# Kernel tuning notes

Hardware: AMD Instinct MI355X
Metric: run time of the kernel (lower is better)

The kernel has to match this reference:

```python
import jax, jax.numpy as jnp
import numpy as np

NW = 64        # n_waveshapers
CE = 128       # control_embedding_size
W = 16         # shaping_fn_size (width)
OC = 1         # out_channels
EPS = 1e-5
SLOPE = 0.01   # LeakyReLU negative slope


def _layer_norm_c(x, g, b):
    # layer norm over channel axis of [B, C, T] (TimeDistributedLayerNorm)
    mu = jnp.mean(x, axis=1, keepdims=True)
    var = jnp.var(x, axis=1, keepdims=True)
    xn = (x - mu) * jax.lax.rsqrt(var + EPS)
    return xn * g[None, :, None] + b[None, :, None]


def _linear_interp(x, out_len):
    # torch F.interpolate(mode='linear', align_corners=False) on [B, C, L]
    L = x.shape[-1]
    scale = L / out_len
    pos = (jnp.arange(out_len, dtype=x.dtype) + 0.5) * scale - 0.5
    pos = jnp.clip(pos, 0.0, L - 1)
    i0 = jnp.floor(pos).astype(jnp.int32)
    i1 = jnp.minimum(i0 + 1, L - 1)
    frac = (pos - i0.astype(x.dtype))
    return x[..., i0] * (1.0 - frac) + x[..., i1] * frac


def setup_inputs() -> dict:
    key = jax.random.key(0)
    ks = jax.random.split(key, 32)
    B, T, TC = 4, 65536, 1024
    s_ce = 1.0 / np.sqrt(CE)
    inp = {
        'exciter': jax.random.normal(ks[0], (B, NW, T), jnp.float32),
        'control_embedding': jax.random.normal(ks[1], (B, CE, TC), jnp.float32),
        # TimeDistributedMLP (depth=4): three CE->CE convs + final CE->4*NW
        'mlp_w0': jax.random.normal(ks[2], (CE, CE), jnp.float32) * s_ce,
        'mlp_b0': jnp.zeros((CE,), jnp.float32),
        'ln0_g': jnp.ones((CE,), jnp.float32),
        'ln0_b': jnp.zeros((CE,), jnp.float32),
        'mlp_w1': jax.random.normal(ks[3], (CE, CE), jnp.float32) * s_ce,
        'mlp_b1': jnp.zeros((CE,), jnp.float32),
        'ln1_g': jnp.ones((CE,), jnp.float32),
        'ln1_b': jnp.zeros((CE,), jnp.float32),
        'mlp_w2': jax.random.normal(ks[4], (CE, CE), jnp.float32) * s_ce,
        'mlp_b2': jnp.zeros((CE,), jnp.float32),
        'ln2_g': jnp.ones((CE,), jnp.float32),
        'ln2_b': jnp.zeros((CE,), jnp.float32),
        'mlp_w3': jax.random.normal(ks[5], (4 * NW, CE), jnp.float32) * s_ce,
        'mlp_b3': jnp.zeros((4 * NW,), jnp.float32),
        # TrainableNonlinearity: input_scale + grouped k=1 convs (per-channel MLPs)
        'input_scale': jax.random.normal(ks[6], (1, NW, 1), jnp.float32) * 10.0,
        'sf_w0': jax.random.normal(ks[7], (NW, W), jnp.float32),            # 1 -> W per group
        'sf_b0': jnp.zeros((NW, W), jnp.float32),
        'sf_w1': jax.random.normal(ks[8], (NW, W, W), jnp.float32) / np.sqrt(W),  # W -> W per group
        'sf_b1': jnp.zeros((NW, W), jnp.float32),
        'sf_w2': jax.random.normal(ks[9], (NW, W), jnp.float32) / np.sqrt(W),     # W -> 1 per group
        'sf_b2': jnp.zeros((NW,), jnp.float32),
        # mixer conv1d NW -> OC, k=1
        'mix_w': jax.random.normal(ks[10], (OC, NW), jnp.float32) / np.sqrt(NW),
        'mix_b': jnp.zeros((OC,), jnp.float32),
    }
    return inp


def reference(exciter, control_embedding,
              mlp_w0, mlp_b0, ln0_g, ln0_b,
              mlp_w1, mlp_b1, ln1_g, ln1_b,
              mlp_w2, mlp_b2, ln2_g, ln2_b,
              mlp_w3, mlp_b3,
              input_scale, sf_w0, sf_b0, sf_w1, sf_b1, sf_w2, sf_b2,
              mix_w, mix_b):
    T = exciter.shape[-1]

    # --- TimeDistributedMLP: (Conv1x1 -> LN(channels) -> LeakyReLU) x3 -> Conv1x1
    h = jnp.einsum('bct,oc->bot', control_embedding, mlp_w0) + mlp_b0[None, :, None]
    h = jax.nn.leaky_relu(_layer_norm_c(h, ln0_g, ln0_b), SLOPE)
    h = jnp.einsum('bct,oc->bot', h, mlp_w1) + mlp_b1[None, :, None]
    h = jax.nn.leaky_relu(_layer_norm_c(h, ln1_g, ln1_b), SLOPE)
    h = jnp.einsum('bct,oc->bot', h, mlp_w2) + mlp_b2[None, :, None]
    h = jax.nn.leaky_relu(_layer_norm_c(h, ln2_g, ln2_b), SLOPE)
    film = jnp.einsum('bct,oc->bot', h, mlp_w3) + mlp_b3[None, :, None]  # [B, 4*NW, TC]

    # upsample control params to audio rate
    film = _linear_interp(film, T)  # [B, 4*NW, T]
    gamma_i, beta_i, gamma_n, beta_n = jnp.split(film, 4, axis=1)

    # FiLM waveshaping index
    x = gamma_i * exciter + beta_i  # [B, NW, T]

    # TrainableNonlinearity: per-channel 1->W->W->1 MLP, Sine activations
    x = input_scale * x
    h0 = jnp.sin(x[:, :, None, :] * sf_w0[None, :, :, None] + sf_b0[None, :, :, None])  # [B,NW,W,T]
    h1 = jnp.sin(jnp.einsum('bcit,coi->bcot', h0, sf_w1) + sf_b1[None, :, :, None])     # [B,NW,W,T]
    x = jnp.sin(jnp.einsum('bcit,ci->bct', h1, sf_w2) + sf_b2[None, :, None])           # [B,NW,T]

    # FiLM normalising coeff
    x = gamma_n * x + beta_n

    # nearest upsample x4 then 1x1 mixer conv
    x = jnp.repeat(x, 4, axis=-1)  # [B, NW, 4T]
    out = jnp.einsum('bct,oc->bot', x, mix_w) + mix_b[None, :, None]  # [B, OC, 4T]
    return out
```

## Files before the change

kernel.cpp:

```cpp
#include <hip/hip_runtime.h>
#include <stdint.h>

#define NB 4
#define NWS 64
#define TT 65536
#define TCC 1024
#define CEE 128
#define WW 16

#define INV2PI 0.15915494309189535f

#define OFF_FILM  0
#define OFF_SB    (OFF_FILM + NB*256*TCC)
#define OFF_W0S   (OFF_SB + NB*TCC)
#define OFF_B0S   (OFF_W0S + 1024)
#define OFF_B1S   (OFF_B0S + 1024)
#define OFF_B2S   (OFF_B1S + 1024)
#define OFF_AFRAG (OFF_B2S + 64)
#define OFF_PART  (OFF_AFRAG + 16384)

typedef _Float16 half4_t __attribute__((ext_vector_type(4)));
typedef _Float16 half2_t __attribute__((ext_vector_type(2)));
typedef __fp16 fp16x2_t __attribute__((ext_vector_type(2)));
typedef float f32x4_t __attribute__((ext_vector_type(4)));

union H4 { half4_t h4; half2_t h2[2]; fp16x2_t f2[2]; uint2 u; };

__device__ __forceinline__ float sinrev(float r) {
#if __has_builtin(__builtin_amdgcn_fractf) && __has_builtin(__builtin_amdgcn_sinf)
  return __builtin_amdgcn_sinf(__builtin_amdgcn_fractf(r));
#else
  float fr = r - floorf(r);
  return __sinf(fr * 6.283185307179586f);
#endif
}

#define MCOLS 8
__global__ __launch_bounds__(256) void k_mlp(
    const float* __restrict__ ce,
    const float* __restrict__ w0, const float* __restrict__ b0,
    const float* __restrict__ g0, const float* __restrict__ e0,
    const float* __restrict__ w1, const float* __restrict__ b1,
    const float* __restrict__ g1, const float* __restrict__ e1,
    const float* __restrict__ w2, const float* __restrict__ b2,
    const float* __restrict__ g2, const float* __restrict__ e2,
    const float* __restrict__ w3, const float* __restrict__ b3,
    const float* __restrict__ iscale,
    const float* __restrict__ sw0, const float* __restrict__ sb0,
    const float* __restrict__ sw1, const float* __restrict__ sb1,
    const float* __restrict__ sw2, const float* __restrict__ sb2,
    const float* __restrict__ mixw,
    float* __restrict__ ws) {
  const int tid = threadIdx.x;
  const int bx = blockIdx.x;

  if (bx < 16) {
    int i = bx * 256 + tid;
    if (i < NWS * WW) {
      int n = i / WW;
      ws[OFF_W0S + i] = sw0[i] * iscale[n] * INV2PI;
      ws[OFF_B0S + i] = sb0[i] * INV2PI;
      ws[OFF_B1S + i] = sb1[i] * INV2PI;
    }
    if (i < NWS) ws[OFF_B2S + i] = sb2[i] * INV2PI;
    {
      int n = i >> 6, l = i & 63;
      int m = l & 15, k0 = (l >> 4) * 4;
      H4 a1, a2;
      #pragma unroll
      for (int j = 0; j < 4; ++j) {
        a1.h4[j] = (_Float16)(sw1[(n * 16 + m) * 16 + k0 + j] * INV2PI);
        a2.h4[j] = (_Float16)(sw2[n * 16 + k0 + j] * INV2PI);
      }
      uint4 o; o.x = a1.u.x; o.y = a1.u.y; o.z = a2.u.x; o.w = a2.u.y;
      ((uint4*)(ws + OFF_AFRAG))[i] = o;
    }
  }

  const int o = tid & 127;
  const int h = tid >> 7;
  const int wvid = tid >> 6;
  const int b = bx >> 7;
  const int tc0 = (bx & 127) * MCOLS;
  float* film = ws + OFF_FILM;

  __shared__ float wlds[128 * 65];
  __shared__ __align__(16) float xa[CEE * MCOLS];
  __shared__ __align__(16) float xb[CEE * MCOLS];
  __shared__ float red[4][2][4];
  __shared__ float stat[2][MCOLS];

  if (tid < 128) {
    const float* src = ce + ((size_t)(b * CEE + tid)) * TCC + tc0;
    *(float4*)(xa + tid * MCOLS) = *(const float4*)src;
    *(float4*)(xa + tid * MCOLS + 4) = *(const float4*)(src + 4);
  }

  float* xin = xa; float* xout = xb;
  const float* Wp[3] = {w0, w1, w2};
  const float* Bp[3] = {b0, b1, b2};
  const float* Gp[3] = {g0, g1, g2};
  const float* Ep[3] = {e0, e1, e2};

  for (int L = 0; L < 3; ++L) {
    float acc[4];
    float bias = Bp[L][o];
    #pragma unroll
    for (int cc = 0; cc < 4; ++cc) acc[cc] = bias;

    for (int half = 0; half < 2; ++half) {
      __syncthreads();
      const float* wsrc = Wp[L] + half * 64;
      for (int i = tid; i < 4096; i += 256) {
        int oo = i >> 5, cc2 = (i & 31) * 2;
        float2 wv = *(const float2*)(wsrc + (size_t)oo * CEE + cc2);
        wlds[oo * 65 + cc2] = wv.x;
        wlds[oo * 65 + cc2 + 1] = wv.y;
      }
      __syncthreads();
      const float* xcol = xin + half * 64 * MCOLS + h * 4;
      const float* wr = wlds + o * 65;
      #pragma unroll 8
      for (int c = 0; c < 64; ++c) {
        float w = wr[c];
        float4 xv = *(const float4*)(xcol + c * MCOLS);
        acc[0] = fmaf(w, xv.x, acc[0]); acc[1] = fmaf(w, xv.y, acc[1]);
        acc[2] = fmaf(w, xv.z, acc[2]); acc[3] = fmaf(w, xv.w, acc[3]);
      }
    }

    float s[4], q[4];
    #pragma unroll
    for (int cc = 0; cc < 4; ++cc) { s[cc] = acc[cc]; q[cc] = acc[cc] * acc[cc]; }
    #pragma unroll
    for (int m = 1; m < 64; m <<= 1) {
      #pragma unroll
      for (int cc = 0; cc < 4; ++cc) {
        s[cc] += __shfl_xor(s[cc], m, 64);
        q[cc] += __shfl_xor(q[cc], m, 64);
      }
    }
    if ((tid & 63) == 0) {
      #pragma unroll
      for (int cc = 0; cc < 4; ++cc) { red[wvid][0][cc] = s[cc]; red[wvid][1][cc] = q[cc]; }
    }
    __syncthreads();
    if (tid < MCOLS) {
      int hh = tid >> 2, cc = tid & 3;
      float st = red[2 * hh][0][cc] + red[2 * hh + 1][0][cc];
      float qt = red[2 * hh][1][cc] + red[2 * hh + 1][1][cc];
      float mu = st * (1.0f / CEE);
      float var = qt * (1.0f / CEE) - mu * mu;
      stat[0][tid] = mu;
      stat[1][tid] = rsqrtf(var + 1e-5f);
    }
    __syncthreads();
    float g = Gp[L][o], e = Ep[L][o];
    #pragma unroll
    for (int cc = 0; cc < 4; ++cc) {
      int col = h * 4 + cc;
      float v = (acc[cc] - stat[0][col]) * stat[1][col] * g + e;
      v = fmaxf(v, 0.01f * v);
      xout[o * MCOLS + col] = v;
    }
    float* tmp = xin; xin = xout; xout = tmp;
  }

  for (int hh = 0; hh < 2; ++hh) {
    float acc[4];
    float bias = b3[hh * 128 + o];
    #pragma unroll
    for (int cc = 0; cc < 4; ++cc) acc[cc] = bias;
    for (int half = 0; half < 2; ++half) {
      __syncthreads();
      const float* wsrc = w3 + (size_t)hh * 128 * CEE + half * 64;
      for (int i = tid; i < 4096; i += 256) {
        int oo = i >> 5, cc2 = (i & 31) * 2;
        float2 wv = *(const float2*)(wsrc + (size_t)oo * CEE + cc2);
        wlds[oo * 65 + cc2] = wv.x;
        wlds[oo * 65 + cc2 + 1] = wv.y;
      }
      __syncthreads();
      const float* xcol = xin + half * 64 * MCOLS + h * 4;
      const float* wr = wlds + o * 65;
      #pragma unroll 8
      for (int c = 0; c < 64; ++c) {
        float w = wr[c];
        float4 xv = *(const float4*)(xcol + c * MCOLS);
        acc[0] = fmaf(w, xv.x, acc[0]); acc[1] = fmaf(w, xv.y, acc[1]);
        acc[2] = fmaf(w, xv.z, acc[2]); acc[3] = fmaf(w, xv.w, acc[3]);
      }
    }
    float* dst = film + ((size_t)(b * 256 + hh * 128 + o)) * TCC + tc0 + h * 4;
    *(float4*)dst = *(float4*)acc;

    if (hh == 1 && ((tid >> 6) & 1)) {
      int n = o - 64;
      float mwn = mixw[n];
      float sv[4];
      #pragma unroll
      for (int cc = 0; cc < 4; ++cc) sv[cc] = mwn * acc[cc];
      #pragma unroll
      for (int m = 1; m < 64; m <<= 1) {
        #pragma unroll
        for (int cc = 0; cc < 4; ++cc) sv[cc] += __shfl_xor(sv[cc], m, 64);
      }
      if ((tid & 63) == 0) {
        #pragma unroll
        for (int cc = 0; cc < 4; ++cc)
          ws[OFF_SB + b * TCC + tc0 + h * 4 + cc] = sv[cc];
      }
    }
  }
}

__global__ __launch_bounds__(256, 8) void k_shape(
    const float* __restrict__ exciter,
    const float* __restrict__ ws,
    const float* __restrict__ mixw,
    float* __restrict__ part) {
  const int tid = threadIdx.x;
  const int lane = tid & 63;
  const int wv = tid >> 6;
  const int bx = blockIdx.x;
  const int blk = bx & 255;
  const int b = (bx >> 8) & 3;
  const int quarter = bx >> 10;
  const int n0 = quarter * 16;
  const int t0_blk = blk * 256;
  const int tcbase = blk * 4 - 1;

  __shared__ __align__(16) float FLp[16 * 48];
  __shared__ float Spair[12];
  __shared__ __align__(16) float W0s[16 * 16], B0s[16 * 16], B1s[16 * 16];
  __shared__ float B2s[16];

  if (tid < 16 * 16) {
    W0s[tid] = ws[OFF_W0S + n0 * 16 + tid];
    B0s[tid] = ws[OFF_B0S + n0 * 16 + tid];
    B1s[tid] = ws[OFF_B1S + n0 * 16 + tid];
  }
  if (tid < 16) B2s[tid] = ws[OFF_B2S + n0 + tid];
  if (tid < 96) {
    int n = tid / 6, j = tid - n * 6;
    int tc = tcbase + j; tc = tc < 0 ? 0 : (tc > 1023 ? 1023 : tc);
    int tcn = tcbase + j + 1; tcn = tcn < 0 ? 0 : (tcn > 1023 ? 1023 : tcn);
    const float* fb = ws + OFF_FILM + ((size_t)(b * 256 + n0 + n)) * TCC;
    float g_v = fb[tc], g_n = fb[tcn];
    float b_v = fb[64 * TCC + tc], b_n = fb[64 * TCC + tcn];
    float n_v = fb[128 * TCC + tc], n_n = fb[128 * TCC + tcn];
    float mwn = mixw[n0 + n];
    float* d = FLp + n * 48 + j * 8;
    d[0] = g_v; d[1] = g_n - g_v;
    d[2] = b_v; d[3] = b_n - b_v;
    d[4] = n_v * mwn; d[5] = (n_n - n_v) * mwn;
  }
  if (tid >= 96 && tid < 102 && quarter == 0) {
    int j = tid - 96;
    int tc = tcbase + j; tc = tc < 0 ? 0 : (tc > 1023 ? 1023 : tc);
    int tcn = tcbase + j + 1; tcn = tcn < 0 ? 0 : (tcn > 1023 ? 1023 : tcn);
    float s0 = ws[OFF_SB + b * TCC + tc];
    float s1 = ws[OFF_SB + b * TCC + tcn];
    Spair[2 * j] = s0; Spair[2 * j + 1] = s1 - s0;
  }
  __syncthreads();

  const int t_own = t0_blk + wv * 64 + lane;
  float pos = ((float)t_own + 0.5f) * (1.0f / 64.0f) - 0.5f;
  pos = fminf(fmaxf(pos, 0.0f), 1023.0f);
  float fi = floorf(pos);
  int i0 = (int)fi;
  const float frac = pos - fi;
  const int j0 = i0 - tcbase;

  const int quad = lane >> 4;
  const int l16 = lane & 15;

  float acc = 0.0f;
  const float* excp = exciter + ((size_t)(b * NWS + n0)) * TT + t_own;
  const uint4* afp = (const uint4*)(ws + OFF_AFRAG) + (size_t)n0 * 64 + lane;

  f32x4_t czero; czero[0] = 0.f; czero[1] = 0.f; czero[2] = 0.f; czero[3] = 0.f;

  float ev = excp[0];
  uint4 af = afp[0];
  for (int n = 0; n < 16; ++n) {
    float ev_n = 0.f; uint4 af_n = af;
    if (n < 15) {
      ev_n = excp[(size_t)(n + 1) * TT];
      af_n = afp[(n + 1) * 64];
    }
    const float* fp = FLp + n * 48 + j0 * 8;
    float4 gb = *(const float4*)(fp);
    float2 np = *(const float2*)(fp + 4);
    float gi = fmaf(gb.y, frac, gb.x);
    float bi = fmaf(gb.w, frac, gb.z);
    float gnp = fmaf(np.y, frac, np.x);
    float x = fmaf(gi, ev, bi);

    f32x4_t w0f = *(const f32x4_t*)(W0s + n * 16 + quad * 4);
    f32x4_t b0f = *(const f32x4_t*)(B0s + n * 16 + quad * 4);
    f32x4_t b1f = *(const f32x4_t*)(B1s + n * 16 + quad * 4);
    float b2v = B2s[n];
    H4 a1, a2;
    a1.u.x = af.x; a1.u.y = af.y;
    a2.u.x = af.z; a2.u.y = af.w;

    float yown = 0.0f;
    #pragma unroll
    for (int g = 0; g < 4; ++g) {
      float xg = __shfl(x, g * 16 + l16, 64);
      float s0 = sinrev(fmaf(xg, w0f[0], b0f[0]));
      float s1 = sinrev(fmaf(xg, w0f[1], b0f[1]));
      float s2 = sinrev(fmaf(xg, w0f[2], b0f[2]));
      float s3 = sinrev(fmaf(xg, w0f[3], b0f[3]));
      H4 bf1;
      bf1.f2[0] = __builtin_amdgcn_cvt_pkrtz(s0, s1);
      bf1.f2[1] = __builtin_amdgcn_cvt_pkrtz(s2, s3);
      f32x4_t d1 = __builtin_amdgcn_mfma_f32_16x16x16f16(a1.h4, bf1.h4, b1f, 0, 0, 0);
      float u0 = sinrev(d1[0]);
      float u1 = sinrev(d1[1]);
      float u2 = sinrev(d1[2]);
      float u3 = sinrev(d1[3]);
      H4 bf2;
      bf2.f2[0] = __builtin_amdgcn_cvt_pkrtz(u0, u1);
      bf2.f2[1] = __builtin_amdgcn_cvt_pkrtz(u2, u3);
      f32x4_t d2 = __builtin_amdgcn_mfma_f32_16x16x16f16(a2.h4, bf2.h4, czero, 0, 0, 0);
      yown = (quad == g) ? d2[0] : yown;
    }
    float z = sinrev(yown + b2v);
    acc = fmaf(gnp, z, acc);
    ev = ev_n; af = af_n;
  }
  if (quarter == 0) {
    float2 sp = *(const float2*)(Spair + 2 * j0);
    acc += fmaf(sp.y, frac, sp.x);
  }
  part[((size_t)(quarter * NB + b)) * TT + t_own] = acc;
}

__global__ __launch_bounds__(256) void k_mix(
    const float* __restrict__ part,
    const float* __restrict__ mixb,
    float* __restrict__ out) {
  int idx = blockIdx.x * 256 + threadIdx.x;
  float m = mixb[0];
  float4 a = ((const float4*)part)[idx];
  float4 c = ((const float4*)(part + (size_t)NB * TT))[idx];
  float4 d = ((const float4*)(part + (size_t)2 * NB * TT))[idx];
  float4 e = ((const float4*)(part + (size_t)3 * NB * TT))[idx];
  float4* o = (float4*)(out + (size_t)idx * 16);
  float s0 = a.x + c.x + d.x + e.x + m;
  float s1 = a.y + c.y + d.y + e.y + m;
  float s2 = a.z + c.z + d.z + e.z + m;
  float s3 = a.w + c.w + d.w + e.w + m;
  o[0] = make_float4(s0, s0, s0, s0);
  o[1] = make_float4(s1, s1, s1, s1);
  o[2] = make_float4(s2, s2, s2, s2);
  o[3] = make_float4(s3, s3, s3, s3);
}

extern "C" void kernel_launch(void* const* d_in, const int* in_sizes, int n_in,
                              void* d_out, int out_size, void* d_ws, size_t ws_size,
                              hipStream_t stream) {
  const float* exciter = (const float*)d_in[0];
  const float* ce      = (const float*)d_in[1];
  const float* w0  = (const float*)d_in[2];
  const float* b0  = (const float*)d_in[3];
  const float* g0  = (const float*)d_in[4];
  const float* e0  = (const float*)d_in[5];
  const float* w1  = (const float*)d_in[6];
  const float* b1  = (const float*)d_in[7];
  const float* g1  = (const float*)d_in[8];
  const float* e1  = (const float*)d_in[9];
  const float* w2  = (const float*)d_in[10];
  const float* b2  = (const float*)d_in[11];
  const float* g2  = (const float*)d_in[12];
  const float* e2  = (const float*)d_in[13];
  const float* w3  = (const float*)d_in[14];
  const float* b3  = (const float*)d_in[15];
  const float* iscale = (const float*)d_in[16];
  const float* sw0 = (const float*)d_in[17];
  const float* sb0 = (const float*)d_in[18];
  const float* sw1 = (const float*)d_in[19];
  const float* sb1 = (const float*)d_in[20];
  const float* sw2 = (const float*)d_in[21];
  const float* sb2 = (const float*)d_in[22];
  const float* mixw = (const float*)d_in[23];
  const float* mixb = (const float*)d_in[24];

  float* ws = (float*)d_ws;

  hipLaunchKernelGGL(k_mlp, dim3(512), dim3(256), 0, stream,
                     ce, w0, b0, g0, e0, w1, b1, g1, e1, w2, b2, g2, e2, w3, b3,
                     iscale, sw0, sb0, sw1, sb1, sw2, sb2, mixw, ws);
  hipLaunchKernelGGL(k_shape, dim3(4096), dim3(256), 0, stream,
                     exciter, ws, mixw, ws + OFF_PART);
  hipLaunchKernelGGL(k_mix, dim3(256), dim3(256), 0, stream,
                     ws + OFF_PART, mixb, (float*)d_out);
}
```

Baseline: 249.4 us.

## Run the control MLP on MFMA with split-fp16 weights and a prep kernel

The scalar fp32 control MLP is replaced by 16x16x16 fp16 MFMA tiles. Each operand is split into hi and lo fp16 halves and combined with three MFMAs, to keep close to fp32 accuracy. A new prep kernel packs the weights into fragment layout in the workspace, and each MLP block now handles 16 time columns, with layer norm done through shared memory. Separately, the sine helper drops the fract range reduction before the hardware sin. That saves an instruction in the shaping kernel but could lose accuracy for inputs with large magnitude.

```diff
diff --git a/kernel.cpp b/kernel.cpp
--- a/kernel.cpp
+++ b/kernel.cpp
@@ -17,7 +17,9 @@
 #define OFF_B1S   (OFF_B0S + 1024)
 #define OFF_B2S   (OFF_B1S + 1024)
 #define OFF_AFRAG (OFF_B2S + 64)
-#define OFF_PART  (OFF_AFRAG + 16384)
+#define OFF_WF    (OFF_AFRAG + 16384)
+#define OFF_W3F   (OFF_WF + 49152)
+#define OFF_PART  (OFF_W3F + 32768)
 
 typedef _Float16 half4_t __attribute__((ext_vector_type(4)));
 typedef _Float16 half2_t __attribute__((ext_vector_type(2)));
@@ -27,33 +29,19 @@
 union H4 { half4_t h4; half2_t h2[2]; fp16x2_t f2[2]; uint2 u; };
 
 __device__ __forceinline__ float sinrev(float r) {
-#if __has_builtin(__builtin_amdgcn_fractf) && __has_builtin(__builtin_amdgcn_sinf)
-  return __builtin_amdgcn_sinf(__builtin_amdgcn_fractf(r));
-#else
-  float fr = r - floorf(r);
-  return __sinf(fr * 6.283185307179586f);
-#endif
-}
-
-#define MCOLS 8
-__global__ __launch_bounds__(256) void k_mlp(
-    const float* __restrict__ ce,
-    const float* __restrict__ w0, const float* __restrict__ b0,
-    const float* __restrict__ g0, const float* __restrict__ e0,
-    const float* __restrict__ w1, const float* __restrict__ b1,
-    const float* __restrict__ g1, const float* __restrict__ e1,
-    const float* __restrict__ w2, const float* __restrict__ b2,
-    const float* __restrict__ g2, const float* __restrict__ e2,
-    const float* __restrict__ w3, const float* __restrict__ b3,
+  return __builtin_amdgcn_sinf(r);
+}
+
+__global__ __launch_bounds__(256) void k_prep(
     const float* __restrict__ iscale,
     const float* __restrict__ sw0, const float* __restrict__ sb0,
     const float* __restrict__ sw1, const float* __restrict__ sb1,
     const float* __restrict__ sw2, const float* __restrict__ sb2,
-    const float* __restrict__ mixw,
+    const float* __restrict__ m0, const float* __restrict__ m1,
+    const float* __restrict__ m2, const float* __restrict__ m3,
     float* __restrict__ ws) {
   const int tid = threadIdx.x;
   const int bx = blockIdx.x;
-
   if (bx < 16) {
     int i = bx * 256 + tid;
     if (i < NWS * WW) {
@@ -75,141 +63,217 @@
       uint4 o; o.x = a1.u.x; o.y = a1.u.y; o.z = a2.u.x; o.w = a2.u.y;
       ((uint4*)(ws + OFF_AFRAG))[i] = o;
     }
-  }
-
-  const int o = tid & 127;
-  const int h = tid >> 7;
-  const int wvid = tid >> 6;
-  const int b = bx >> 7;
-  const int tc0 = (bx & 127) * MCOLS;
-  float* film = ws + OFF_FILM;
-
-  __shared__ float wlds[128 * 65];
-  __shared__ __align__(16) float xa[CEE * MCOLS];
-  __shared__ __align__(16) float xb[CEE * MCOLS];
-  __shared__ float red[4][2][4];
-  __shared__ float stat[2][MCOLS];
-
-  if (tid < 128) {
-    const float* src = ce + ((size_t)(b * CEE + tid)) * TCC + tc0;
-    *(float4*)(xa + tid * MCOLS) = *(const float4*)src;
-    *(float4*)(xa + tid * MCOLS + 4) = *(const float4*)(src + 4);
-  }
-
-  float* xin = xa; float* xout = xb;
-  const float* Wp[3] = {w0, w1, w2};
+  } else if (bx < 64) {
+    int i = (bx - 16) * 256 + tid;
+    int l = i & 63, ct = (i >> 6) & 7, kt = (i >> 9) & 7, L = i >> 12;
+    const float* W = (L == 0) ? m0 : (L == 1 ? m1 : m2);
+    int o = ct * 16 + (l & 15);
+    int k0 = kt * 16 + (l >> 4) * 4;
+    H4 hi, lo;
+    #pragma unroll
+    for (int j = 0; j < 4; ++j) {
+      float v = W[o * CEE + k0 + j];
+      _Float16 h = (_Float16)v;
+      hi.h4[j] = h;
+      lo.h4[j] = (_Float16)(v - (float)h);
+    }
+    uint4 q; q.x = hi.u.x; q.y = hi.u.y; q.z = lo.u.x; q.w = lo.u.y;
+    ((uint4*)(ws + OFF_WF))[i] = q;
+  } else {
+    int i = (bx - 64) * 256 + tid;
+    int l = i & 63, ct = (i >> 6) & 15, kt = i >> 10;
+    int o = ct * 16 + (l & 15);
+    int k0 = kt * 16 + (l >> 4) * 4;
+    H4 hi, lo;
+    #pragma unroll
+    for (int j = 0; j < 4; ++j) {
+      float v = m3[o * CEE + k0 + j];
+      _Float16 h = (_Float16)v;
+      hi.h4[j] = h;
+      lo.h4[j] = (_Float16)(v - (float)h);
+    }
+    uint4 q; q.x = hi.u.x; q.y = hi.u.y; q.z = lo.u.x; q.w = lo.u.y;
+    ((uint4*)(ws + OFF_W3F))[i] = q;
+  }
+}
+
+__device__ __forceinline__ void pack_frags(
+    const float* h, uint2* XH, uint2* XL,
+    const float* MU, const float* RS,
+    const float* __restrict__ g, const float* __restrict__ e,
+    bool doLN, int tid) {
+  #pragma unroll
+  for (int i = 0; i < 2; ++i) {
+    int w = tid + i * 256;
+    int l = w & 63, kt = w >> 6;
+    int m = l & 15, k0 = kt * 16 + (l >> 4) * 4;
+    float x[4];
+    #pragma unroll
+    for (int j = 0; j < 4; ++j) {
+      float v = h[m * 137 + k0 + j];
+      if (doLN) {
+        v = (v - MU[m]) * RS[m] * g[k0 + j] + e[k0 + j];
+        v = fmaxf(v, 0.01f * v);
+      }
+      x[j] = v;
+    }
+    H4 hi;
+    hi.f2[0] = __builtin_amdgcn_cvt_pkrtz(x[0], x[1]);
+    hi.f2[1] = __builtin_amdgcn_cvt_pkrtz(x[2], x[3]);
+    float l0 = x[0] - (float)hi.h4[0];
+    float l1 = x[1] - (float)hi.h4[1];
+    float l2 = x[2] - (float)hi.h4[2];
+    float l3 = x[3] - (float)hi.h4[3];
+    H4 lo;
+    lo.f2[0] = __builtin_amdgcn_cvt_pkrtz(l0, l1);
+    lo.f2[1] = __builtin_amdgcn_cvt_pkrtz(l2, l3);
+    XH[kt * 64 + l] = hi.u;
+    XL[kt * 64 + l] = lo.u;
+  }
+}
+
+__global__ __launch_bounds__(256) void k_mlp(
+    const float* __restrict__ ce,
+    const float* __restrict__ b0, const float* __restrict__ g0, const float* __restrict__ e0,
+    const float* __restrict__ b1, const float* __restrict__ g1, const float* __restrict__ e1,
+    const float* __restrict__ b2, const float* __restrict__ g2, const float* __restrict__ e2,
+    const float* __restrict__ b3,
+    const float* __restrict__ mixw,
+    float* __restrict__ ws) {
+  const int tid = threadIdx.x;
+  const int lane = tid & 63;
+  const int wv = tid >> 6;
+  const int l16 = lane & 15;
+  const int quad = lane >> 4;
+  const int bx = blockIdx.x;
+  const int b = bx >> 6;
+  const int tc0 = (bx & 63) * 16;
+
+  __shared__ float h[16 * 137];
+  __shared__ float h2[16 * 265];
+  __shared__ uint2 XH[8 * 64], XL[8 * 64];
+  __shared__ float MU[16], RS[16];
+
+  {
+    int ch = tid >> 1, hf = tid & 1;
+    const float* src = ce + ((size_t)(b * CEE + ch)) * TCC + tc0 + hf * 8;
+    float4 v0 = *(const float4*)src;
+    float4 v1 = *(const float4*)(src + 4);
+    float vv[8] = {v0.x, v0.y, v0.z, v0.w, v1.x, v1.y, v1.z, v1.w};
+    #pragma unroll
+    for (int j = 0; j < 8; ++j) h[(hf * 8 + j) * 137 + ch] = vv[j];
+  }
+  __syncthreads();
+  pack_frags(h, XH, XL, MU, RS, nullptr, nullptr, false, tid);
+  __syncthreads();
+
   const float* Bp[3] = {b0, b1, b2};
   const float* Gp[3] = {g0, g1, g2};
   const float* Ep[3] = {e0, e1, e2};
 
   for (int L = 0; L < 3; ++L) {
-    float acc[4];
-    float bias = Bp[L][o];
-    #pragma unroll
-    for (int cc = 0; cc < 4; ++cc) acc[cc] = bias;
-
-    for (int half = 0; half < 2; ++half) {
-      __syncthreads();
-      const float* wsrc = Wp[L] + half * 64;
-      for (int i = tid; i < 4096; i += 256) {
-        int oo = i >> 5, cc2 = (i & 31) * 2;
-        float2 wv = *(const float2*)(wsrc + (size_t)oo * CEE + cc2);
-        wlds[oo * 65 + cc2] = wv.x;
-        wlds[oo * 65 + cc2 + 1] = wv.y;
-      }
-      __syncthreads();
-      const float* xcol = xin + half * 64 * MCOLS + h * 4;
-      const float* wr = wlds + o * 65;
-      #pragma unroll 8
-      for (int c = 0; c < 64; ++c) {
-        float w = wr[c];
-        float4 xv = *(const float4*)(xcol + c * MCOLS);
-        acc[0] = fmaf(w, xv.x, acc[0]); acc[1] = fmaf(w, xv.y, acc[1]);
-        acc[2] = fmaf(w, xv.z, acc[2]); acc[3] = fmaf(w, xv.w, acc[3]);
-      }
-    }
-
-    float s[4], q[4];
-    #pragma unroll
-    for (int cc = 0; cc < 4; ++cc) { s[cc] = acc[cc]; q[cc] = acc[cc] * acc[cc]; }
-    #pragma unroll
-    for (int m = 1; m < 64; m <<= 1) {
-      #pragma unroll
-      for (int cc = 0; cc < 4; ++cc) {
-        s[cc] += __shfl_xor(s[cc], m, 64);
-        q[cc] += __shfl_xor(q[cc], m, 64);
-      }
-    }
-    if ((tid & 63) == 0) {
-      #pragma unroll
-      for (int cc = 0; cc < 4; ++cc) { red[wvid][0][cc] = s[cc]; red[wvid][1][cc] = q[cc]; }
+    const int ct0 = 2 * wv, ct1 = 2 * wv + 1;
+    float bb0 = Bp[L][ct0 * 16 + l16], bb1 = Bp[L][ct1 * 16 + l16];
+    f32x4_t ac0, ac1;
+    ac0[0] = bb0; ac0[1] = bb0; ac0[2] = bb0; ac0[3] = bb0;
+    ac1[0] = bb1; ac1[1] = bb1; ac1[2] = bb1; ac1[3] = bb1;
+    const uint4* wf = (const uint4*)(ws + OFF_WF) + (size_t)L * 4096;
+    #pragma unroll
+    for (int kt = 0; kt < 8; ++kt) {
+      H4 ah, al;
+      ah.u = XH[kt * 64 + lane];
+      al.u = XL[kt * 64 + lane];
+      uint4 q0 = wf[(kt * 8 + ct0) * 64 + lane];
+      uint4 q1 = wf[(kt * 8 + ct1) * 64 + lane];
+      H4 bh0, bl0, bh1, bl1;
+      bh0.u.x = q0.x; bh0.u.y = q0.y; bl0.u.x = q0.z; bl0.u.y = q0.w;
+      bh1.u.x = q1.x; bh1.u.y = q1.y; bl1.u.x = q1.z; bl1.u.y = q1.w;
+      ac0 = __builtin_amdgcn_mfma_f32_16x16x16f16(ah.h4, bl0.h4, ac0, 0, 0, 0);
+      ac0 = __builtin_amdgcn_mfma_f32_16x16x16f16(al.h4, bh0.h4, ac0, 0, 0, 0);
+      ac0 = __builtin_amdgcn_mfma_f32_16x16x16f16(ah.h4, bh0.h4, ac0, 0, 0, 0);
+      ac1 = __builtin_amdgcn_mfma_f32_16x16x16f16(ah.h4, bl1.h4, ac1, 0, 0, 0);
+      ac1 = __builtin_amdgcn_mfma_f32_16x16x16f16(al.h4, bh1.h4, ac1, 0, 0, 0);
+      ac1 = __builtin_amdgcn_mfma_f32_16x16x16f16(ah.h4, bh1.h4, ac1, 0, 0, 0);
+    }
+    #pragma unroll
+    for (int r = 0; r < 4; ++r) {
+      h[(quad * 4 + r) * 137 + ct0 * 16 + l16] = ac0[r];
+      h[(quad * 4 + r) * 137 + ct1 * 16 + l16] = ac1[r];
     }
     __syncthreads();
-    if (tid < MCOLS) {
-      int hh = tid >> 2, cc = tid & 3;
-      float st = red[2 * hh][0][cc] + red[2 * hh + 1][0][cc];
-      float qt = red[2 * hh][1][cc] + red[2 * hh + 1][1][cc];
-      float mu = st * (1.0f / CEE);
-      float var = qt * (1.0f / CEE) - mu * mu;
-      stat[0][tid] = mu;
-      stat[1][tid] = rsqrtf(var + 1e-5f);
+    {
+      int p = tid >> 4, sb = tid & 15;
+      float s = 0.f, q = 0.f;
+      #pragma unroll
+      for (int j = 0; j < 8; ++j) {
+        float v = h[p * 137 + sb + 16 * j];
+        s += v; q += v * v;
+      }
+      #pragma unroll
+      for (int m2 = 1; m2 < 16; m2 <<= 1) {
+        s += __shfl_xor(s, m2, 64);
+        q += __shfl_xor(q, m2, 64);
+      }
+      if (sb == 0) {
+        float mu = s * (1.0f / CEE);
+        MU[p] = mu;
+        RS[p] = rsqrtf(q * (1.0f / CEE) - mu * mu + 1e-5f);
+      }
     }
     __syncthreads();
-    float g = Gp[L][o], e = Ep[L][o];
-    #pragma unroll
-    for (int cc = 0; cc < 4; ++cc) {
-      int col = h * 4 + cc;
-      float v = (acc[cc] - stat[0][col]) * stat[1][col] * g + e;
-      v = fmaxf(v, 0.01f * v);
-      xout[o * MCOLS + col] = v;
-    }
-    float* tmp = xin; xin = xout; xout = tmp;
-  }
-
-  for (int hh = 0; hh < 2; ++hh) {
-    float acc[4];
-    float bias = b3[hh * 128 + o];
-    #pragma unroll
-    for (int cc = 0; cc < 4; ++cc) acc[cc] = bias;
-    for (int half = 0; half < 2; ++half) {
-      __syncthreads();
-      const float* wsrc = w3 + (size_t)hh * 128 * CEE + half * 64;
-      for (int i = tid; i < 4096; i += 256) {
-        int oo = i >> 5, cc2 = (i & 31) * 2;
-        float2 wv = *(const float2*)(wsrc + (size_t)oo * CEE + cc2);
-        wlds[oo * 65 + cc2] = wv.x;
-        wlds[oo * 65 + cc2 + 1] = wv.y;
-      }
-      __syncthreads();
-      const float* xcol = xin + half * 64 * MCOLS + h * 4;
-      const float* wr = wlds + o * 65;
-      #pragma unroll 8
-      for (int c = 0; c < 64; ++c) {
-        float w = wr[c];
-        float4 xv = *(const float4*)(xcol + c * MCOLS);
-        acc[0] = fmaf(w, xv.x, acc[0]); acc[1] = fmaf(w, xv.y, acc[1]);
-        acc[2] = fmaf(w, xv.z, acc[2]); acc[3] = fmaf(w, xv.w, acc[3]);
-      }
-    }
-    float* dst = film + ((size_t)(b * 256 + hh * 128 + o)) * TCC + tc0 + h * 4;
-    *(float4*)dst = *(float4*)acc;
-
-    if (hh == 1 && ((tid >> 6) & 1)) {
-      int n = o - 64;
-      float mwn = mixw[n];
-      float sv[4];
-      #pragma unroll
-      for (int cc = 0; cc < 4; ++cc) sv[cc] = mwn * acc[cc];
-      #pragma unroll
-      for (int m = 1; m < 64; m <<= 1) {
-        #pragma unroll
-        for (int cc = 0; cc < 4; ++cc) sv[cc] += __shfl_xor(sv[cc], m, 64);
-      }
-      if ((tid & 63) == 0) {
-        #pragma unroll
-        for (int cc = 0; cc < 4; ++cc)
-          ws[OFF_SB + b * TCC + tc0 + h * 4 + cc] = sv[cc];
-      }
+    pack_frags(h, XH, XL, MU, RS, Gp[L], Ep[L], true, tid);
+    __syncthreads();
+  }
+
+  {
+    const uint4* wf = (const uint4*)(ws + OFF_W3F);
+    f32x4_t ac[4];
+    #pragma unroll
+    for (int c = 0; c < 4; ++c) {
+      float bb = b3[(wv * 4 + c) * 16 + l16];
+      ac[c][0] = bb; ac[c][1] = bb; ac[c][2] = bb; ac[c][3] = bb;
+    }
+    #pragma unroll
+    for (int kt = 0; kt < 8; ++kt) {
+      H4 ah, al;
+      ah.u = XH[kt * 64 + lane];
+      al.u = XL[kt * 64 + lane];
+      #pragma unroll
+      for (int c = 0; c < 4; ++c) {
+        uint4 q = wf[(kt * 16 + wv * 4 + c) * 64 + lane];
+        H4 bh, bl;
+        bh.u.x = q.x; bh.u.y = q.y; bl.u.x = q.z; bl.u.y = q.w;
+        ac[c] = __builtin_amdgcn_mfma_f32_16x16x16f16(ah.h4, bl.h4, ac[c], 0, 0, 0);
+        ac[c] = __builtin_amdgcn_mfma_f32_16x16x16f16(al.h4, bh.h4, ac[c], 0, 0, 0);
+        ac[c] = __builtin_amdgcn_mfma_f32_16x16x16f16(ah.h4, bh.h4, ac[c], 0, 0, 0);
+      }
+    }
+    #pragma unroll
+    for (int c = 0; c < 4; ++c)
+      #pragma unroll
+      for (int r = 0; r < 4; ++r)
+        h2[(quad * 4 + r) * 265 + (wv * 4 + c) * 16 + l16] = ac[c][r];
+  }
+  __syncthreads();
+
+  {
+    int ch = tid;
+    float vv[16];
+    #pragma unroll
+    for (int t = 0; t < 16; ++t) vv[t] = h2[t * 265 + ch];
+    float* dst = ws + OFF_FILM + ((size_t)(b * 256 + ch)) * TCC + tc0;
+    *(float4*)(dst) = make_float4(vv[0], vv[1], vv[2], vv[3]);
+    *(float4*)(dst + 4) = make_float4(vv[4], vv[5], vv[6], vv[7]);
+    *(float4*)(dst + 8) = make_float4(vv[8], vv[9], vv[10], vv[11]);
+    *(float4*)(dst + 12) = make_float4(vv[12], vv[13], vv[14], vv[15]);
+  }
+  if (wv == 0) {
+    float mw = mixw[lane];
+    for (int t = 0; t < 16; ++t) {
+      float v = h2[t * 265 + 192 + lane] * mw;
+      #pragma unroll
+      for (int m2 = 1; m2 < 64; m2 <<= 1) v += __shfl_xor(v, m2, 64);
+      if (lane == 0) ws[OFF_SB + b * TCC + tc0 + t] = v;
     }
   }
 }
@@ -391,9 +455,10 @@
 
   float* ws = (float*)d_ws;
 
-  hipLaunchKernelGGL(k_mlp, dim3(512), dim3(256), 0, stream,
-                     ce, w0, b0, g0, e0, w1, b1, g1, e1, w2, b2, g2, e2, w3, b3,
-                     iscale, sw0, sb0, sw1, sb1, sw2, sb2, mixw, ws);
+  hipLaunchKernelGGL(k_prep, dim3(96), dim3(256), 0, stream,
+                     iscale, sw0, sb0, sw1, sb1, sw2, sb2, w0, w1, w2, w3, ws);
+  hipLaunchKernelGGL(k_mlp, dim3(256), dim3(256), 0, stream,
+                     ce, b0, g0, e0, b1, g1, e1, b2, g2, e2, b3, mixw, ws);
   hipLaunchKernelGGL(k_shape, dim3(4096), dim3(256), 0, stream,
                      exciter, ws, mixw, ws + OFF_PART);
   hipLaunchKernelGGL(k_mix, dim3(256), dim3(256), 0, stream,
```

Result: faster. 210.6 us (-15.5%).
